# Optimization experiments

Hardware: AMD Instinct MI355X
Metric: run time of the kernel (lower is better)

## Reference

```python
import math
import jax, jax.numpy as jnp
import numpy as np
from jax import lax

D_MODEL = 1024
D_STATE = 8
D_CONV = 4
EXPAND = 2
D_INNER = EXPAND * D_MODEL          # 2048
DT_RANK = math.ceil(D_MODEL / 16)   # 64
R_RANK = 8
BATCH, SEQLEN = 2, 4096


def setup_inputs() -> dict:
    key = jax.random.key(0)
    ks = jax.random.split(key, 12)
    hidden_states = jax.random.normal(ks[0], (BATCH, SEQLEN, D_MODEL), dtype=jnp.float32)
    # parameters
    in_proj_w = jax.random.normal(ks[1], (2 * D_INNER, D_MODEL), dtype=jnp.float32) * (D_MODEL ** -0.5)
    conv_w = jax.random.normal(ks[2], (D_INNER, D_CONV), dtype=jnp.float32) * (D_CONV ** -0.5)
    conv_b = jax.random.normal(ks[3], (D_INNER,), dtype=jnp.float32) * 0.02
    x_proj_w = jax.random.normal(ks[4], (DT_RANK + 2 * D_STATE, D_INNER), dtype=jnp.float32) * (D_INNER ** -0.5)
    dt_init_std = DT_RANK ** -0.5
    dt_proj_w = jax.random.uniform(ks[5], (D_INNER, DT_RANK), minval=-dt_init_std, maxval=dt_init_std, dtype=jnp.float32)
    # dt bias: inverse-softplus of dt sampled log-uniform in [1e-3, 1e-1]
    dt = jnp.exp(jax.random.uniform(ks[6], (D_INNER,)) * (math.log(0.1) - math.log(0.001)) + math.log(0.001))
    dt = jnp.clip(dt, 1e-4, None)
    dt_proj_b = dt + jnp.log(-jnp.expm1(-dt))
    A_log = jnp.log(jnp.broadcast_to(jnp.arange(1, D_STATE + 1, dtype=jnp.float32), (D_INNER, D_STATE)))
    D = jnp.ones((D_INNER,), dtype=jnp.float32)
    out_proj_w = jax.random.normal(ks[7], (D_MODEL, D_INNER), dtype=jnp.float32) * (D_INNER ** -0.5)
    U_param = jax.random.normal(ks[8], (D_INNER, R_RANK), dtype=jnp.float32) * 0.02
    V_param = jax.random.normal(ks[9], (R_RANK, D_STATE), dtype=jnp.float32) * 0.02
    low_rank_scale = jnp.float32(0.05)
    return dict(hidden_states=hidden_states, in_proj_w=in_proj_w, conv_w=conv_w,
                conv_b=conv_b, x_proj_w=x_proj_w, dt_proj_w=dt_proj_w,
                dt_proj_b=dt_proj_b, A_log=A_log, D=D, out_proj_w=out_proj_w,
                U_param=U_param, V_param=V_param, low_rank_scale=low_rank_scale)


def _silu(x):
    return x * jax.nn.sigmoid(x)


def _mamba_fwd(hidden_states, in_proj_w, conv_w, conv_b, x_proj_w, dt_proj_w,
               dt_proj_b, A_log, D, out_proj_w, U_param, V_param, low_rank_scale):
    b, l, _ = hidden_states.shape
    # in_proj: (b,l,d_model) -> (b, 2*d_inner, l)
    xz = jnp.einsum('bld,ed->bel', hidden_states, in_proj_w)
    x, z = xz[:, :D_INNER], xz[:, D_INNER:]               # (b, d_inner, l) each
    # causal depthwise conv1d (torch pads both sides d_conv-1 then slices [:l])
    xp = jnp.pad(x, ((0, 0), (0, 0), (D_CONV - 1, 0)))
    x = lax.conv_general_dilated(xp, conv_w[:, None, :], (1,), 'VALID',
                                 dimension_numbers=('NCH', 'OIH', 'NCH'),
                                 feature_group_count=D_INNER)
    x = _silu(x + conv_b[None, :, None])                  # (b, d_inner, l)
    # x_proj -> dt, B, C
    x_dbl = jnp.einsum('bdl,kd->blk', x, x_proj_w)        # (b, l, dt_rank+2n)
    dt_lr = x_dbl[..., :DT_RANK]
    B = x_dbl[..., DT_RANK:DT_RANK + D_STATE]             # (b, l, n)
    C = x_dbl[..., DT_RANK + D_STATE:]                    # (b, l, n)
    dt = jnp.einsum('blr,dr->bld', dt_lr, dt_proj_w)      # (b, l, d_inner)
    # A with static low-rank correction
    A = -jnp.exp(A_log) + low_rank_scale * (U_param @ V_param) / math.sqrt(R_RANK)
    delta = jax.nn.softplus(dt + dt_proj_b[None, None, :])  # (b, l, d_inner)
    # selective scan (sequential recurrence over time)
    u = jnp.swapaxes(x, 1, 2)                             # (b, l, d_inner)
    xs = (jnp.swapaxes(delta, 0, 1), jnp.swapaxes(B, 0, 1),
          jnp.swapaxes(u, 0, 1), jnp.swapaxes(C, 0, 1))   # each (l, b, ...)
    h0 = jnp.zeros((b, D_INNER, D_STATE), dtype=jnp.float32)

    def step(h, t):
        dlt, Bt, ut, Ct = t                                # (b,d), (b,n), (b,d), (b,n)
        dA = jnp.exp(dlt[..., None] * A)                   # (b, d, n)
        h = h * dA + (dlt * ut)[..., None] * Bt[:, None, :]
        y = jnp.einsum('bdn,bn->bd', h, Ct)
        return h, y

    _, ys = lax.scan(step, h0, xs)                        # (l, b, d_inner)
    y = jnp.swapaxes(ys, 0, 1)                            # (b, l, d_inner)
    y = y + u * D[None, None, :]                          # D skip
    y = y * _silu(jnp.swapaxes(z, 1, 2))                  # gate
    return jnp.einsum('bld,md->blm', y, out_proj_w)       # (b, l, d_model)


def reference(hidden_states, in_proj_w, conv_w, conv_b, x_proj_w, dt_proj_w,
              dt_proj_b, A_log, D, out_proj_w, U_param, V_param, low_rank_scale):
    return _mamba_fwd(hidden_states, in_proj_w, conv_w, conv_b, x_proj_w,
                      dt_proj_w, dt_proj_b, A_log, D, out_proj_w, U_param,
                      V_param, low_rank_scale)
```

## Files before the change

kernel.cpp:

```cpp
#include <hip/hip_runtime.h>
#include <hip/hip_bf16.h>
#include <math.h>


#define BATCH   2
#define SEQLEN  4096
#define DMODEL  1024
#define DINNER  2048
#define E2      4096
#define DSTATE  8
#define DTRANK  64
#define NK      80
#define BL      (BATCH * SEQLEN)
#define CHUNK   64
#define NCHUNK  (SEQLEN / CHUNK)
#define LOG2E   1.44269504088896341f

typedef short bf16x8 __attribute__((ext_vector_type(8)));
typedef float f32x4  __attribute__((ext_vector_type(4)));
typedef unsigned short ushort8 __attribute__((ext_vector_type(8)));

__device__ __forceinline__ unsigned short f2bf(float f) {
    unsigned u = __float_as_uint(f);
    u += 0x7FFF + ((u >> 16) & 1);
    return (unsigned short)(u >> 16);
}
__device__ __forceinline__ float bf2f(unsigned short h) {
    return __uint_as_float((unsigned)h << 16);
}
__device__ __forceinline__ float fexp2(float x) {
    float r;
    asm("v_exp_f32 %0, %1" : "=v"(r) : "v"(x));
    return r;
}
__device__ __forceinline__ float frcp(float x) {
    float r;
    asm("v_rcp_f32 %0, %1" : "=v"(r) : "v"(x));
    return r;
}

__global__ __launch_bounds__(256) void split_kernel(
    const float* __restrict__ src,
    unsigned short* __restrict__ hi, unsigned short* __restrict__ lo, int n4)
{
    int i = blockIdx.x * 256 + threadIdx.x;
    if (i >= n4) return;
    float4 v = ((const float4*)src)[i];
    ushort4 h, l;
    h.x = f2bf(v.x); h.y = f2bf(v.y); h.z = f2bf(v.z); h.w = f2bf(v.w);
    l.x = f2bf(v.x - bf2f(h.x)); l.y = f2bf(v.y - bf2f(h.y));
    l.z = f2bf(v.z - bf2f(h.z)); l.w = f2bf(v.w - bf2f(h.w));
    ((ushort4*)hi)[i] = h;
    ((ushort4*)lo)[i] = l;
}

#define LDSW 32

__device__ __forceinline__ int swz(int row, int col_u) {
    return ((row << 5) + col_u) ^ ((row & 7) << 3);
}

template <int APK, int SPLITC>
__global__ __launch_bounds__(256) void gemm_bf3p(
    const unsigned short* __restrict__ Ah_g,
    const unsigned short* __restrict__ Al_g, int lda,
    const unsigned short* __restrict__ Bh_g,
    const unsigned short* __restrict__ Bl_g, int ldb,
    float* __restrict__ C0, float* __restrict__ C1, int ldc,
    int N, int K)
{
    __shared__ unsigned short Ah[128 * LDSW], Al[128 * LDSW];
    __shared__ unsigned short Bh[128 * LDSW], Bl[128 * LDSW];

    const int tid  = threadIdx.x;
    const int lane = tid & 63;
    const int wave = tid >> 6;
    const int bm   = blockIdx.y << 7;
    const int bn   = blockIdx.x << 7;

    const int sr = tid >> 2;
    const int sc = (tid & 3) << 3;

    const int pr = tid >> 3;
    const int pc = (tid & 7) << 2;

    const int wm = (wave >> 1) << 6;
    const int wn = (wave & 1) << 6;
    const int fr = lane & 15;
    const int kg = lane >> 4;

    f32x4 acc[4][4];
#pragma unroll
    for (int i = 0; i < 4; ++i)
#pragma unroll
        for (int j = 0; j < 4; ++j)
            acc[i][j] = (f32x4){0.f, 0.f, 0.f, 0.f};

    const ushort8 zz = {0, 0, 0, 0, 0, 0, 0, 0};

    for (int k0 = 0; k0 < K; k0 += 32) {
        ushort8 a_h[2], a_l[2], b_h[2], b_l[2];
        ushort4 p_h[4], p_l[4];

        if (APK == 0) {
#pragma unroll
            for (int s = 0; s < 2; ++s) {
                size_t ao = (size_t)(bm + sr + s * 64) * lda + k0 + sc;
                a_h[s] = *(const ushort8*)&Ah_g[ao];
                a_l[s] = *(const ushort8*)&Al_g[ao];
            }
        } else {
            const unsigned* Apk = (const unsigned*)Ah_g;
#pragma unroll
            for (int s = 0; s < 4; ++s) {
                size_t ao = (size_t)(bm + pr + s * 32) * lda + k0 + pc;
                uint4 pk = *(const uint4*)&Apk[ao];
                p_h[s].x = (unsigned short)(pk.x >> 16);
                p_h[s].y = (unsigned short)(pk.y >> 16);
                p_h[s].z = (unsigned short)(pk.z >> 16);
                p_h[s].w = (unsigned short)(pk.w >> 16);
                p_l[s].x = (unsigned short)(pk.x & 0xffff);
                p_l[s].y = (unsigned short)(pk.y & 0xffff);
                p_l[s].z = (unsigned short)(pk.z & 0xffff);
                p_l[s].w = (unsigned short)(pk.w & 0xffff);
            }
        }
#pragma unroll
        for (int s = 0; s < 2; ++s) {
            int r = bn + sr + s * 64;
            if (r < N) {
                size_t bo = (size_t)r * ldb + k0 + sc;
                b_h[s] = *(const ushort8*)&Bh_g[bo];
                b_l[s] = *(const ushort8*)&Bl_g[bo];
            } else {
                b_h[s] = zz; b_l[s] = zz;
            }
        }

        __syncthreads();
        if (APK == 0) {
#pragma unroll
            for (int s = 0; s < 2; ++s) {
                const int o = swz(sr + s * 64, sc);
                *(ushort8*)&Ah[o] = a_h[s];
                *(ushort8*)&Al[o] = a_l[s];
            }
        } else {
#pragma unroll
            for (int s = 0; s < 4; ++s) {
                const int o = swz(pr + s * 32, pc);
                *(ushort4*)&Ah[o] = p_h[s];
                *(ushort4*)&Al[o] = p_l[s];
            }
        }
#pragma unroll
        for (int s = 0; s < 2; ++s) {
            const int o = swz(sr + s * 64, sc);
            *(ushort8*)&Bh[o] = b_h[s];
            *(ushort8*)&Bl[o] = b_l[s];
        }
        __syncthreads();

        bf16x8 fa_h[4], fa_l[4], fb_h[4], fb_l[4];
#pragma unroll
        for (int f = 0; f < 4; ++f) {
            const int ra = swz(wm + f * 16 + fr, kg << 3);
            const int rb = swz(wn + f * 16 + fr, kg << 3);
            fa_h[f] = *(const bf16x8*)&Ah[ra];
            fa_l[f] = *(const bf16x8*)&Al[ra];
            fb_h[f] = *(const bf16x8*)&Bh[rb];
            fb_l[f] = *(const bf16x8*)&Bl[rb];
        }

#pragma unroll
        for (int i = 0; i < 4; ++i)
#pragma unroll
            for (int j = 0; j < 4; ++j) {
                acc[i][j] = __builtin_amdgcn_mfma_f32_16x16x32_bf16(
                    fa_h[i], fb_h[j], acc[i][j], 0, 0, 0);
                acc[i][j] = __builtin_amdgcn_mfma_f32_16x16x32_bf16(
                    fa_l[i], fb_h[j], acc[i][j], 0, 0, 0);
                acc[i][j] = __builtin_amdgcn_mfma_f32_16x16x32_bf16(
                    fa_h[i], fb_l[j], acc[i][j], 0, 0, 0);
            }
    }

    const int erow = (lane >> 4) << 2;
    const int ecol = lane & 15;
    float* Cw = C0;
    int cb = bn;
    if (SPLITC && bn >= DINNER) { Cw = C1; cb = bn - DINNER; }
#pragma unroll
    for (int i = 0; i < 4; ++i) {
        const int row0 = bm + wm + i * 16 + erow;
#pragma unroll
        for (int j = 0; j < 4; ++j) {
            const int col = wn + j * 16 + ecol;
            if (bn + col < N) {
#pragma unroll
                for (int r = 0; r < 4; ++r)
                    Cw[(size_t)(row0 + r) * ldc + cb + col] = acc[i][j][r];
            }
        }
    }
}

__global__ __launch_bounds__(256) void gemm_nt_sp(
    const float* __restrict__ A, int lda,
    const float* __restrict__ B, int ldb,
    const float* __restrict__ bias,
    float* __restrict__ C, int ldc,
    int N, int K)
{
    __shared__ float As[16][64];
    __shared__ float Bs[16][64];

    const int tid  = threadIdx.x;
    const int tx   = tid & 15;
    const int ty   = tid >> 4;
    const int bm   = blockIdx.y << 6;
    const int bn   = blockIdx.x << 6;
    const int lrow = tid >> 2;
    const int lcol = (tid & 3) << 2;

    const float* Aptr = A + (size_t)(bm + lrow) * lda + lcol;
    const float* Bptr = B + (size_t)(bn + lrow) * ldb + lcol;
    const bool   bval = (bn + lrow) < N;

    float acc[4][4] = {};

    for (int k0 = 0; k0 < K; k0 += 16) {
        float4 av = *(const float4*)(Aptr + k0);
        float4 bv = make_float4(0.f, 0.f, 0.f, 0.f);
        if (bval) bv = *(const float4*)(Bptr + k0);

        __syncthreads();
        As[lcol + 0][lrow] = av.x;
        As[lcol + 1][lrow] = av.y;
        As[lcol + 2][lrow] = av.z;
        As[lcol + 3][lrow] = av.w;
        Bs[lcol + 0][lrow] = bv.x;
        Bs[lcol + 1][lrow] = bv.y;
        Bs[lcol + 2][lrow] = bv.z;
        Bs[lcol + 3][lrow] = bv.w;
        __syncthreads();

#pragma unroll
        for (int kk = 0; kk < 16; ++kk) {
            float4 a4 = *(const float4*)&As[kk][ty << 2];
            float4 b4 = *(const float4*)&Bs[kk][tx << 2];
            float ar[4] = {a4.x, a4.y, a4.z, a4.w};
            float br[4] = {b4.x, b4.y, b4.z, b4.w};
#pragma unroll
            for (int i = 0; i < 4; ++i)
#pragma unroll
                for (int j = 0; j < 4; ++j)
                    acc[i][j] = fmaf(ar[i], br[j], acc[i][j]);
        }
    }

    const int cm = bm + (ty << 2);
    const int cn = bn + (tx << 2);
#pragma unroll
    for (int i = 0; i < 4; ++i) {
#pragma unroll
        for (int j = 0; j < 4; ++j) {
            int nn = cn + j;
            if (nn < N) {
                float v = acc[i][j] + bias[nn];
                v = (v > 20.f) ? v : log1pf(expf(v));
                C[(size_t)(cm + i) * ldc + nn] = v;
            }
        }
    }
}

__global__ __launch_bounds__(256) void a_eff_kernel(
    const float* __restrict__ A_log, const float* __restrict__ U,
    const float* __restrict__ V, const float* __restrict__ scale_p,
    float* __restrict__ Aeff2)
{
    int d = blockIdx.x * 256 + threadIdx.x;
    if (d >= DINNER) return;
    const float s = (*scale_p) * 0.35355339059327378f;
    float ur[8];
#pragma unroll
    for (int r = 0; r < 8; ++r) ur[r] = U[d * 8 + r];
#pragma unroll
    for (int n = 0; n < DSTATE; ++n) {
        float acc = 0.f;
#pragma unroll
        for (int r = 0; r < 8; ++r) acc = fmaf(ur[r], V[r * 8 + n], acc);
        Aeff2[d * 8 + n] = (-expf(A_log[d * 8 + n]) + s * acc) * LOG2E;
    }
}

__global__ __launch_bounds__(256) void conv_silu_kernel(
    const float* __restrict__ xbuf, const float* __restrict__ cw,
    const float* __restrict__ cb,
    unsigned short* __restrict__ xth, unsigned short* __restrict__ xtl)
{
    const int d = blockIdx.x * 256 + threadIdx.x;
    const int l = blockIdx.y;
    const int b = blockIdx.z;

    float4 w = *(const float4*)&cw[d * 4];
    size_t idx = ((size_t)b * SEQLEN + l) * DINNER + d;

    float acc = cb[d];
    if (l >= 3) acc = fmaf(w.x, xbuf[idx - 3 * (size_t)DINNER], acc);
    if (l >= 2) acc = fmaf(w.y, xbuf[idx - 2 * (size_t)DINNER], acc);
    if (l >= 1) acc = fmaf(w.z, xbuf[idx - 1 * (size_t)DINNER], acc);
    acc = fmaf(w.w, xbuf[idx], acc);

    float sig = 1.f / (1.f + expf(-acc));
    float v = acc * sig;
    unsigned short h = f2bf(v);
    xth[idx] = h;
    xtl[idx] = f2bf(v - bf2f(h));
}

__global__ __launch_bounds__(256) void scan_phase1(
    const float* __restrict__ delta,
    const unsigned short* __restrict__ uh,
    const unsigned short* __restrict__ ul,
    const float* __restrict__ xdbl,
    const float* __restrict__ Aeff2,
    float* __restrict__ P, float* __restrict__ S)
{
    const int d = blockIdx.x * 256 + threadIdx.x;
    const int c = blockIdx.y;
    const int b = blockIdx.z;

    const float4 a0 = *(const float4*)&Aeff2[d * 8];
    const float4 a1 = *(const float4*)&Aeff2[d * 8 + 4];

    float4 s0 = make_float4(0.f, 0.f, 0.f, 0.f);
    float4 s1 = make_float4(0.f, 0.f, 0.f, 0.f);
    float sdl = 0.f;

    size_t rowD = ((size_t)b * SEQLEN + (size_t)c * CHUNK) * DINNER + d;
    size_t rowX = ((size_t)b * SEQLEN + (size_t)c * CHUNK) * NK + DTRANK;

    for (int t = 0; t < CHUNK; ++t) {
        float dl = delta[rowD];
        float ut = bf2f(uh[rowD]) + bf2f(ul[rowD]);
        float4 B0 = *(const float4*)&xdbl[rowX];
        float4 B1 = *(const float4*)&xdbl[rowX + 4];
        float dlut = dl * ut;

        s0.x = fmaf(s0.x, fexp2(dl * a0.x), dlut * B0.x);
        s0.y = fmaf(s0.y, fexp2(dl * a0.y), dlut * B0.y);
        s0.z = fmaf(s0.z, fexp2(dl * a0.z), dlut * B0.z);
        s0.w = fmaf(s0.w, fexp2(dl * a0.w), dlut * B0.w);
        s1.x = fmaf(s1.x, fexp2(dl * a1.x), dlut * B1.x);
        s1.y = fmaf(s1.y, fexp2(dl * a1.y), dlut * B1.y);
        s1.z = fmaf(s1.z, fexp2(dl * a1.z), dlut * B1.z);
        s1.w = fmaf(s1.w, fexp2(dl * a1.w), dlut * B1.w);

        sdl += dl;
        rowD += DINNER; rowX += NK;
    }

    size_t idx = (((size_t)b * NCHUNK + c) * DINNER + d) * 8;
    float4 p0 = make_float4(fexp2(sdl * a0.x), fexp2(sdl * a0.y),
                            fexp2(sdl * a0.z), fexp2(sdl * a0.w));
    float4 p1 = make_float4(fexp2(sdl * a1.x), fexp2(sdl * a1.y),
                            fexp2(sdl * a1.z), fexp2(sdl * a1.w));
    *(float4*)&P[idx]     = p0;
    *(float4*)&P[idx + 4] = p1;
    *(float4*)&S[idx]     = s0;
    *(float4*)&S[idx + 4] = s1;
}

__global__ __launch_bounds__(256) void scan_combine(
    float* __restrict__ P, const float* __restrict__ S)
{
    const int i = blockIdx.x * 256 + threadIdx.x;
    if (i >= BATCH * DINNER * DSTATE) return;
    const int b  = i / (DINNER * DSTATE);
    const int dn = i - b * (DINNER * DSTATE);

    float running = 0.f;
    for (int c = 0; c < NCHUNK; ++c) {
        size_t idx = (size_t)(b * NCHUNK + c) * (DINNER * DSTATE) + dn;
        float Pc = P[idx];
        float Sc = S[idx];
        P[idx] = running;
        running = fmaf(running, Pc, Sc);
    }
}

__global__ __launch_bounds__(256) void scan_phase2(
    float* __restrict__ deltay,
    const unsigned short* __restrict__ uh,
    const unsigned short* __restrict__ ul,
    const float* __restrict__ xdbl,
    const float* __restrict__ zbuf,
    const float* __restrict__ Aeff2,
    const float* __restrict__ Dvec,
    const float* __restrict__ H0)
{
    const int d = blockIdx.x * 256 + threadIdx.x;
    const int c = blockIdx.y;
    const int b = blockIdx.z;

    const float4 a0 = *(const float4*)&Aeff2[d * 8];
    const float4 a1 = *(const float4*)&Aeff2[d * 8 + 4];
    const float  Dd = Dvec[d];

    size_t hidx = (((size_t)b * NCHUNK + c) * DINNER + d) * 8;
    float4 h0 = *(const float4*)&H0[hidx];
    float4 h1 = *(const float4*)&H0[hidx + 4];

    size_t rowD = ((size_t)b * SEQLEN + (size_t)c * CHUNK) * DINNER + d;
    size_t rowX = ((size_t)b * SEQLEN + (size_t)c * CHUNK) * NK + DTRANK;

    for (int t = 0; t < CHUNK; ++t) {
        float dl = deltay[rowD];
        float ut = bf2f(uh[rowD]) + bf2f(ul[rowD]);
        float zt = zbuf[rowD];
        float4 B0 = *(const float4*)&xdbl[rowX];
        float4 B1 = *(const float4*)&xdbl[rowX + 4];
        float4 C0 = *(const float4*)&xdbl[rowX + 8];
        float4 C1 = *(const float4*)&xdbl[rowX + 12];
        float dlut = dl * ut;

        h0.x = fmaf(h0.x, fexp2(dl * a0.x), dlut * B0.x);
        h0.y = fmaf(h0.y, fexp2(dl * a0.y), dlut * B0.y);
        h0.z = fmaf(h0.z, fexp2(dl * a0.z), dlut * B0.z);
        h0.w = fmaf(h0.w, fexp2(dl * a0.w), dlut * B0.w);
        h1.x = fmaf(h1.x, fexp2(dl * a1.x), dlut * B1.x);
        h1.y = fmaf(h1.y, fexp2(dl * a1.y), dlut * B1.y);
        h1.z = fmaf(h1.z, fexp2(dl * a1.z), dlut * B1.z);
        h1.w = fmaf(h1.w, fexp2(dl * a1.w), dlut * B1.w);

        float p = h0.x * C0.x;
        p = fmaf(h0.y, C0.y, p);
        p = fmaf(h0.z, C0.z, p);
        p = fmaf(h0.w, C0.w, p);
        p = fmaf(h1.x, C1.x, p);
        p = fmaf(h1.y, C1.y, p);
        p = fmaf(h1.z, C1.z, p);
        p = fmaf(h1.w, C1.w, p);

        float sig = frcp(1.f + fexp2(-zt * LOG2E));
        float yv = (p + ut * Dd) * (zt * sig);
        unsigned short yhi = f2bf(yv);
        unsigned short ylo = f2bf(yv - bf2f(yhi));
        ((unsigned*)deltay)[rowD] = ((unsigned)yhi << 16) | ylo;

        rowD += DINNER; rowX += NK;
    }
}

extern "C" void kernel_launch(void* const* d_in, const int* in_sizes, int n_in,
                              void* d_out, int out_size, void* d_ws, size_t ws_size,
                              hipStream_t stream)
{
    const float* hidden     = (const float*)d_in[0];
    const float* in_proj_w  = (const float*)d_in[1];
    const float* conv_w     = (const float*)d_in[2];
    const float* conv_b     = (const float*)d_in[3];
    const float* x_proj_w   = (const float*)d_in[4];
    const float* dt_proj_w  = (const float*)d_in[5];
    const float* dt_proj_b  = (const float*)d_in[6];
    const float* A_log      = (const float*)d_in[7];
    const float* Dvec       = (const float*)d_in[8];
    const float* out_proj_w = (const float*)d_in[9];
    const float* U_param    = (const float*)d_in[10];
    const float* V_param    = (const float*)d_in[11];
    const float* scale_p    = (const float*)d_in[12];
    float* out = (float*)d_out;

    float* xbuf = (float*)d_ws;
    float* zbuf = xbuf + (size_t)BL * DINNER;
    unsigned short* xth = (unsigned short*)(zbuf + (size_t)BL * DINNER);
    unsigned short* xtl = xth + (size_t)BL * DINNER;

    unsigned short* ipwh = xth;
    unsigned short* ipwl = xth + (size_t)E2 * DMODEL;

    unsigned short* hidh = (unsigned short*)out;
    unsigned short* hidl = hidh + (size_t)BL * DMODEL;
    float* xdbl = out;
    float* Aeff = xdbl + (size_t)BL * NK;
    float* Parr = Aeff + (size_t)DINNER * DSTATE;
    float* Sarr = Parr + (size_t)BATCH * NCHUNK * DINNER * DSTATE;
    unsigned short* xpwh = (unsigned short*)(Sarr + (size_t)BATCH * NCHUNK * DINNER * DSTATE);
    unsigned short* xpwl = xpwh + (size_t)NK * DINNER;

    unsigned short* opwh = (unsigned short*)zbuf;
    unsigned short* opwl = opwh + (size_t)DMODEL * DINNER;

    split_kernel<<<dim3(BL * DMODEL / 1024), 256, 0, stream>>>(
        hidden, hidh, hidl, BL * DMODEL / 4);
    split_kernel<<<dim3(E2 * DMODEL / 1024), 256, 0, stream>>>(
        in_proj_w, ipwh, ipwl, E2 * DMODEL / 4);

    gemm_bf3p<0, 1><<<dim3(E2 / 128, BL / 128), 256, 0, stream>>>(
        hidh, hidl, DMODEL, ipwh, ipwl, DMODEL,
        xbuf, zbuf, DINNER, E2, DMODEL);

    a_eff_kernel<<<dim3(DINNER / 256), 256, 0, stream>>>(
        A_log, U_param, V_param, scale_p, Aeff);
    split_kernel<<<dim3(NK * DINNER / 1024), 256, 0, stream>>>(
        x_proj_w, xpwh, xpwl, NK * DINNER / 4);

    conv_silu_kernel<<<dim3(DINNER / 256, SEQLEN, BATCH), 256, 0, stream>>>(
        xbuf, conv_w, conv_b, xth, xtl);

    gemm_bf3p<0, 0><<<dim3(1, BL / 128), 256, 0, stream>>>(
        xth, xtl, DINNER, xpwh, xpwl, DINNER,
        xdbl, nullptr, NK, NK, DINNER);

    gemm_nt_sp<<<dim3(DINNER / 64, BL / 64), 256, 0, stream>>>(
        xdbl, NK, dt_proj_w, DTRANK, dt_proj_b, xbuf, DINNER, DINNER, DTRANK);

    scan_phase1<<<dim3(DINNER / 256, NCHUNK, BATCH), 256, 0, stream>>>(
        xbuf, xth, xtl, xdbl, Aeff, Parr, Sarr);
    scan_combine<<<dim3((BATCH * DINNER * DSTATE + 255) / 256), 256, 0, stream>>>(
        Parr, Sarr);
    scan_phase2<<<dim3(DINNER / 256, NCHUNK, BATCH), 256, 0, stream>>>(
        xbuf, xth, xtl, xdbl, zbuf, Aeff, Dvec, Parr);

    split_kernel<<<dim3(DMODEL * DINNER / 1024), 256, 0, stream>>>(
        out_proj_w, opwh, opwl, DMODEL * DINNER / 4);

    gemm_bf3p<1, 0><<<dim3(DMODEL / 128, BL / 128), 256, 0, stream>>>(
        (const unsigned short*)xbuf, nullptr, DINNER, opwh, opwl, DINNER,
        out, nullptr, DMODEL, DMODEL, DINNER);
}
```

Before: 718.8 us.

## Pre-pack weights into MFMA fragment layout and load B directly from global

Weight matrices are split into bf16 hi/lo parts and written in a layout that matches the MFMA B-fragment lane order, so each wave can load its B fragments straight from global memory into registers. This removes the B staging through LDS (stores, loads and half the shared memory) in all three bf3p GEMMs. The tradeoff is that B tiles are no longer shared across the two waves in a block row, so each wave fetches its own B data from global/L2, which raises global traffic while easing LDS pressure and possibly improving occupancy.

Measured after the change: 710.1 us. About the same (-1.2%).

```diff
diff --git a/kernel.cpp b/kernel.cpp
--- a/kernel.cpp
+++ b/kernel.cpp
@@ -54,6 +54,33 @@
     ((ushort4*)lo)[i] = l;
 }
 
+__global__ __launch_bounds__(256) void split_frag_kernel(
+    const float* __restrict__ src,
+    unsigned short* __restrict__ hi, unsigned short* __restrict__ lo,
+    int K, int nthreads)
+{
+    int t = blockIdx.x * 256 + threadIdx.x;
+    if (t >= nthreads) return;
+    const int ko = K >> 3;
+    int n = t / ko;
+    int k = (t - n * ko) << 3;
+
+    const float4* s = (const float4*)(src + (size_t)n * K + k);
+    float4 v0 = s[0], v1 = s[1];
+    float vv[8] = {v0.x, v0.y, v0.z, v0.w, v1.x, v1.y, v1.z, v1.w};
+    ushort8 h, l;
+#pragma unroll
+    for (int j = 0; j < 8; ++j) {
+        unsigned short hb = f2bf(vv[j]);
+        h[j] = hb;
+        l[j] = f2bf(vv[j] - bf2f(hb));
+    }
+    const int lane = (n & 15) + (((k >> 3) & 3) << 4);
+    size_t addr = (((size_t)(n >> 4) * (K >> 5) + (k >> 5)) << 9) + lane * 8;
+    *(ushort8*)&hi[addr] = h;
+    *(ushort8*)&lo[addr] = l;
+}
+
 #define LDSW 32
 
 __device__ __forceinline__ int swz(int row, int col_u) {
@@ -64,19 +91,19 @@
 __global__ __launch_bounds__(256) void gemm_bf3p(
     const unsigned short* __restrict__ Ah_g,
     const unsigned short* __restrict__ Al_g, int lda,
-    const unsigned short* __restrict__ Bh_g,
-    const unsigned short* __restrict__ Bl_g, int ldb,
+    const unsigned short* __restrict__ Bfh,
+    const unsigned short* __restrict__ Bfl,
     float* __restrict__ C0, float* __restrict__ C1, int ldc,
     int N, int K)
 {
     __shared__ unsigned short Ah[128 * LDSW], Al[128 * LDSW];
-    __shared__ unsigned short Bh[128 * LDSW], Bl[128 * LDSW];
 
     const int tid  = threadIdx.x;
     const int lane = tid & 63;
     const int wave = tid >> 6;
     const int bm   = blockIdx.y << 7;
     const int bn   = blockIdx.x << 7;
+    const int KT   = K >> 5;
 
     const int sr = tid >> 2;
     const int sc = (tid & 3) << 3;
@@ -96,12 +123,25 @@
         for (int j = 0; j < 4; ++j)
             acc[i][j] = (f32x4){0.f, 0.f, 0.f, 0.f};
 
-    const ushort8 zz = {0, 0, 0, 0, 0, 0, 0, 0};
+    const bf16x8 zb = {0, 0, 0, 0, 0, 0, 0, 0};
+    const int nf0 = (bn + wn) >> 4;
 
     for (int k0 = 0; k0 < K; k0 += 32) {
-        ushort8 a_h[2], a_l[2], b_h[2], b_l[2];
+        bf16x8 fb_h[4], fb_l[4];
+#pragma unroll
+        for (int f = 0; f < 4; ++f) {
+            if (bn + wn + f * 16 < N) {
+                size_t ad = (((size_t)(nf0 + f) * KT + (k0 >> 5)) << 9)
+                          + (size_t)lane * 8;
+                fb_h[f] = *(const bf16x8*)&Bfh[ad];
+                fb_l[f] = *(const bf16x8*)&Bfl[ad];
+            } else {
+                fb_h[f] = zb; fb_l[f] = zb;
+            }
+        }
+
+        ushort8 a_h[2], a_l[2];
         ushort4 p_h[4], p_l[4];
-
         if (APK == 0) {
 #pragma unroll
             for (int s = 0; s < 2; ++s) {
@@ -125,17 +165,6 @@
                 p_l[s].w = (unsigned short)(pk.w & 0xffff);
             }
         }
-#pragma unroll
-        for (int s = 0; s < 2; ++s) {
-            int r = bn + sr + s * 64;
-            if (r < N) {
-                size_t bo = (size_t)r * ldb + k0 + sc;
-                b_h[s] = *(const ushort8*)&Bh_g[bo];
-                b_l[s] = *(const ushort8*)&Bl_g[bo];
-            } else {
-                b_h[s] = zz; b_l[s] = zz;
-            }
-        }
 
         __syncthreads();
         if (APK == 0) {
@@ -153,23 +182,14 @@
                 *(ushort4*)&Al[o] = p_l[s];
             }
         }
-#pragma unroll
-        for (int s = 0; s < 2; ++s) {
-            const int o = swz(sr + s * 64, sc);
-            *(ushort8*)&Bh[o] = b_h[s];
-            *(ushort8*)&Bl[o] = b_l[s];
-        }
         __syncthreads();
 
-        bf16x8 fa_h[4], fa_l[4], fb_h[4], fb_l[4];
+        bf16x8 fa_h[4], fa_l[4];
 #pragma unroll
         for (int f = 0; f < 4; ++f) {
             const int ra = swz(wm + f * 16 + fr, kg << 3);
-            const int rb = swz(wn + f * 16 + fr, kg << 3);
             fa_h[f] = *(const bf16x8*)&Ah[ra];
             fa_l[f] = *(const bf16x8*)&Al[ra];
-            fb_h[f] = *(const bf16x8*)&Bh[rb];
-            fb_l[f] = *(const bf16x8*)&Bl[rb];
         }
 
 #pragma unroll
@@ -495,23 +515,23 @@
 
     split_kernel<<<dim3(BL * DMODEL / 1024), 256, 0, stream>>>(
         hidden, hidh, hidl, BL * DMODEL / 4);
-    split_kernel<<<dim3(E2 * DMODEL / 1024), 256, 0, stream>>>(
-        in_proj_w, ipwh, ipwl, E2 * DMODEL / 4);
+    split_frag_kernel<<<dim3(E2 * DMODEL / 8 / 256), 256, 0, stream>>>(
+        in_proj_w, ipwh, ipwl, DMODEL, E2 * DMODEL / 8);
 
     gemm_bf3p<0, 1><<<dim3(E2 / 128, BL / 128), 256, 0, stream>>>(
-        hidh, hidl, DMODEL, ipwh, ipwl, DMODEL,
+        hidh, hidl, DMODEL, ipwh, ipwl,
         xbuf, zbuf, DINNER, E2, DMODEL);
 
     a_eff_kernel<<<dim3(DINNER / 256), 256, 0, stream>>>(
         A_log, U_param, V_param, scale_p, Aeff);
-    split_kernel<<<dim3(NK * DINNER / 1024), 256, 0, stream>>>(
-        x_proj_w, xpwh, xpwl, NK * DINNER / 4);
+    split_frag_kernel<<<dim3(NK * DINNER / 8 / 256), 256, 0, stream>>>(
+        x_proj_w, xpwh, xpwl, DINNER, NK * DINNER / 8);
 
     conv_silu_kernel<<<dim3(DINNER / 256, SEQLEN, BATCH), 256, 0, stream>>>(
         xbuf, conv_w, conv_b, xth, xtl);
 
     gemm_bf3p<0, 0><<<dim3(1, BL / 128), 256, 0, stream>>>(
-        xth, xtl, DINNER, xpwh, xpwl, DINNER,
+        xth, xtl, DINNER, xpwh, xpwl,
         xdbl, nullptr, NK, NK, DINNER);
 
     gemm_nt_sp<<<dim3(DINNER / 64, BL / 64), 256, 0, stream>>>(
@@ -524,10 +544,10 @@
     scan_phase2<<<dim3(DINNER / 256, NCHUNK, BATCH), 256, 0, stream>>>(
         xbuf, xth, xtl, xdbl, zbuf, Aeff, Dvec, Parr);
 
-    split_kernel<<<dim3(DMODEL * DINNER / 1024), 256, 0, stream>>>(
-        out_proj_w, opwh, opwl, DMODEL * DINNER / 4);
+    split_frag_kernel<<<dim3(DMODEL * DINNER / 8 / 256), 256, 0, stream>>>(
+        out_proj_w, opwh, opwl, DINNER, DMODEL * DINNER / 8);
 
     gemm_bf3p<1, 0><<<dim3(DMODEL / 128, BL / 128), 256, 0, stream>>>(
-        (const unsigned short*)xbuf, nullptr, DINNER, opwh, opwl, DINNER,
+        (const unsigned short*)xbuf, nullptr, DINNER, opwh, opwl,
         out, nullptr, DMODEL, DMODEL, DINNER);
 }
```
